# Optimization experiments

Measured on AMD Instinct MI355X. Metric: run time of the kernel, lower is better.

Reference implementation:

```python
import jax, jax.numpy as jnp
import numpy as np


def setup_inputs() -> dict:
    key = jax.random.key(0)
    ks = jax.random.split(key, 16)
    L, T, F = 1024, 4096, 8
    E, H, P = 4, 4, 4
    return {
        "x": jax.random.normal(ks[0], (L, T, F), jnp.float32),
        "emb": jax.random.normal(ks[1], (L, E), jnp.float32),
        "W1": jax.random.normal(ks[2], (F + E, 4), jnp.float32) * 0.3,
        "b1": jnp.zeros((4,), jnp.float32),
        "Wp": jax.random.normal(ks[3], (4, P), jnp.float32) * 0.3,
        "bp": jnp.zeros((P,), jnp.float32),
        "Wi": jax.random.normal(ks[4], (P, H), jnp.float32) * 0.3,
        "bi": jnp.zeros((H,), jnp.float32),
        "Wh": jax.random.normal(ks[5], (H, H), jnp.float32) * 0.3,
        "Wo1": jax.random.normal(ks[6], (H, 6), jnp.float32) * 0.3,
        "bo1": jnp.zeros((6,), jnp.float32),
        "Wo2": jax.random.normal(ks[7], (6, 1), jnp.float32) * 0.3,
        "bo2": jnpp if False else jnp.zeros((1,), jnp.float32),
    }


def reference(x, emb, W1, b1, Wp, bp, Wi, bi, Wh, Wo1, bo1, Wo2, bo2):
    L, T, F = x.shape
    # location embedding broadcast over time, concat on feature axis -> [L, T, F+E]
    loc = jnp.broadcast_to(emb[:, None, :], (L, T, emb.shape[-1]))
    h = jnp.concatenate([x, loc], axis=-1)
    # pre layers (dropout is identity, training=False)
    h = jax.nn.relu(h @ W1 + b1)          # [L, T, 4]
    h = h @ Wp + bp                        # [L, T, P]
    # SimpleCell RNN: carry = tanh(x_t @ Wi + bi + carry @ Wh), zero init carry
    xs = jnp.swapaxes(h, 0, 1)             # [T, L, P]
    pre = xs @ Wi + bi                     # precompute input projection [T, L, H]
    c0 = jnp.zeros((L, Wh.shape[0]), h.dtype)

    def step(c, p_t):
        c = jnp.tanh(p_t + c @ Wh)
        return c, c

    _, ys = jax.lax.scan(step, c0, pre)    # ys: [T, L, H]
    y = jnp.swapaxes(ys, 0, 1)             # [L, T, H]
    y = jax.nn.relu(y @ Wo1 + bo1)
    y = y @ Wo2 + bo2                      # [L, T, 1]
    return y
```

## Files before the change

### kernel.cpp

```cpp
#include <hip/hip_runtime.h>


#define TSTEP 8

__device__ __forceinline__ float tanh_from_s(float s) {
    float e = __builtin_amdgcn_exp2f(s);
    float r = __builtin_amdgcn_rcpf(e + 1.0f);
    return fmaf(-2.0f, r, 1.0f);
}

__global__ __launch_bounds__(256) void k_fused(
    const float* __restrict__ x, const float* __restrict__ emb,
    const float* __restrict__ W1, const float* __restrict__ b1,
    const float* __restrict__ Wp, const float* __restrict__ bp,
    const float* __restrict__ Wi, const float* __restrict__ bi,
    const float* __restrict__ Wh, const float* __restrict__ Wo1,
    const float* __restrict__ bo1, const float* __restrict__ Wo2,
    const float* __restrict__ bo2, float* __restrict__ out,
    int L, int T, int C, int S, int W)
{
    int wk = blockIdx.x * blockDim.x + threadIdx.x;
    int l = wk % L;
    int k = wk / L;
    if (k >= C) return;

    const float K2 = 2.8853900817779268f;

    float w1[48];
#pragma unroll
    for (int i = 0; i < 48; i++) w1[i] = W1[i];

    float wc[16], bc[4];
#pragma unroll
    for (int a = 0; a < 4; a++)
#pragma unroll
        for (int h = 0; h < 4; h++) {
            float s = 0.f;
#pragma unroll
            for (int p = 0; p < 4; p++) s = fmaf(Wp[a * 4 + p], Wi[p * 4 + h], s);
            wc[a * 4 + h] = s * K2;
        }
#pragma unroll
    for (int h = 0; h < 4; h++) {
        float s = bi[h];
#pragma unroll
        for (int p = 0; p < 4; p++) s = fmaf(bp[p], Wi[p * 4 + h], s);
        bc[h] = s * K2;
    }
    float wh[16];
#pragma unroll
    for (int i = 0; i < 16; i++) wh[i] = Wh[i] * K2;
    float wo1[24], vbo1[6], wo2[6];
#pragma unroll
    for (int i = 0; i < 24; i++) wo1[i] = Wo1[i];
#pragma unroll
    for (int i = 0; i < 6; i++) { vbo1[i] = bo1[i]; wo2[i] = Wo2[i]; }
    float vbo2 = bo2[0];

    float eb[4];
    {
        float e0 = emb[l * 4 + 0], e1 = emb[l * 4 + 1];
        float e2 = emb[l * 4 + 2], e3 = emb[l * 4 + 3];
#pragma unroll
        for (int j = 0; j < 4; j++) {
            float s = b1[j];
            s = fmaf(e0, w1[8 * 4 + j], s);
            s = fmaf(e1, w1[9 * 4 + j], s);
            s = fmaf(e2, w1[10 * 4 + j], s);
            s = fmaf(e3, w1[11 * 4 + j], s);
            eb[j] = s;
        }
    }

    int tmain = k * S;
    int warm = (W < tmain) ? W : tmain;
    int tstart = tmain - warm;

    const float4* xp = (const float4*)x + ((long)l * T + tstart) * 2;
    float c0 = 0.f, c1 = 0.f, c2 = 0.f, c3 = 0.f;

    auto step = [&](const float4& Aa, const float4& Bb) {
        float xf[8] = {Aa.x, Aa.y, Aa.z, Aa.w, Bb.x, Bb.y, Bb.z, Bb.w};
        float hj[4];
#pragma unroll
        for (int j = 0; j < 4; j++) {
            float s = eb[j];
#pragma unroll
            for (int i = 0; i < 8; i++) s = fmaf(xf[i], w1[i * 4 + j], s);
            hj[j] = fmaxf(s, 0.f);
        }
        float p0 = bc[0], p1 = bc[1], p2 = bc[2], p3 = bc[3];
#pragma unroll
        for (int a = 0; a < 4; a++) {
            p0 = fmaf(hj[a], wc[a * 4 + 0], p0);
            p1 = fmaf(hj[a], wc[a * 4 + 1], p1);
            p2 = fmaf(hj[a], wc[a * 4 + 2], p2);
            p3 = fmaf(hj[a], wc[a * 4 + 3], p3);
        }
        p0 = fmaf(c0, wh[0], p0);  p1 = fmaf(c0, wh[1], p1);  p2 = fmaf(c0, wh[2], p2);  p3 = fmaf(c0, wh[3], p3);
        p0 = fmaf(c1, wh[4], p0);  p1 = fmaf(c1, wh[5], p1);  p2 = fmaf(c1, wh[6], p2);  p3 = fmaf(c1, wh[7], p3);
        p0 = fmaf(c2, wh[8], p0);  p1 = fmaf(c2, wh[9], p1);  p2 = fmaf(c2, wh[10], p2); p3 = fmaf(c2, wh[11], p3);
        p0 = fmaf(c3, wh[12], p0); p1 = fmaf(c3, wh[13], p1); p2 = fmaf(c3, wh[14], p2); p3 = fmaf(c3, wh[15], p3);
        c0 = tanh_from_s(p0); c1 = tanh_from_s(p1);
        c2 = tanh_from_s(p2); c3 = tanh_from_s(p3);
    };
    auto outv = [&]() -> float {
        float acc = vbo2;
#pragma unroll
        for (int m = 0; m < 6; m++) {
            float g = vbo1[m];
            g = fmaf(c0, wo1[0 * 6 + m], g);
            g = fmaf(c1, wo1[1 * 6 + m], g);
            g = fmaf(c2, wo1[2 * 6 + m], g);
            g = fmaf(c3, wo1[3 * 6 + m], g);
            acc = fmaf(fmaxf(g, 0.f), wo2[m], acc);
        }
        return acc;
    };

    int wtiles = warm / TSTEP;
    for (int wt = 0; wt < wtiles; wt++) {
        float4 xd[2 * TSTEP];
#pragma unroll
        for (int i = 0; i < 2 * TSTEP; i++) xd[i] = xp[i];
        xp += 2 * TSTEP;
#pragma unroll
        for (int i = 0; i < TSTEP; i++) step(xd[2 * i], xd[2 * i + 1]);
    }

    float* op = out + (long)l * T + tmain;
    int mtiles = S / TSTEP;
    for (int mt = 0; mt < mtiles; mt++) {
        float4 xd[2 * TSTEP];
#pragma unroll
        for (int i = 0; i < 2 * TSTEP; i++) xd[i] = xp[i];
        xp += 2 * TSTEP;
        float o8[TSTEP];
#pragma unroll
        for (int i = 0; i < TSTEP; i++) {
            step(xd[2 * i], xd[2 * i + 1]);
            o8[i] = outv();
        }
        *(float4*)(op + 0) = make_float4(o8[0], o8[1], o8[2], o8[3]);
        *(float4*)(op + 4) = make_float4(o8[4], o8[5], o8[6], o8[7]);
        op += TSTEP;
    }
}

extern "C" void kernel_launch(void* const* d_in, const int* in_sizes, int n_in,
                              void* d_out, int out_size, void* d_ws, size_t ws_size,
                              hipStream_t stream) {
    const float* x   = (const float*)d_in[0];
    const float* emb = (const float*)d_in[1];
    const float* W1  = (const float*)d_in[2];
    const float* b1  = (const float*)d_in[3];
    const float* Wp  = (const float*)d_in[4];
    const float* bp  = (const float*)d_in[5];
    const float* Wi  = (const float*)d_in[6];
    const float* bi  = (const float*)d_in[7];
    const float* Wh  = (const float*)d_in[8];
    const float* Wo1 = (const float*)d_in[9];
    const float* bo1 = (const float*)d_in[10];
    const float* Wo2 = (const float*)d_in[11];
    const float* bo2 = (const float*)d_in[12];
    float* out = (float*)d_out;

    int L = in_sizes[1] / 4;
    int T = (int)(in_sizes[0] / ((long)L * 8));

    int C = 64, W = 48;
    if (T % (C * TSTEP) != 0) { C = 1; W = 0; }
    int S = T / C;

    long nw = (long)L * C;
    int tb = 256;
    int nb = (int)((nw + tb - 1) / tb);
    k_fused<<<nb, tb, 0, stream>>>(x, emb, W1, b1, Wp, bp, Wi, bi, Wh,
                                   Wo1, bo1, Wo2, bo2, out, L, T, C, S, W);
}
```

Measured before the change: 47.88 us.

## Add LDS-staged scan kernel with coalesced x loads and transposed output stores

Adds a new kernel with 64-thread blocks, one block per 64 locations and time chunk. Each 8-step tile of x is loaded cooperatively so that 16 lanes read contiguous memory per row, staged through padded LDS, and then each lane reads its own row. The next tile is prefetched into registers during compute. Outputs are also staged through LDS and written coalesced. This replaces strided per-thread float4 loads at the cost of barriers and low occupancy (launch_bounds 64,1). The fallback kernel picks up a typo (p3 instead of p2 in one FMA), but that path does not run for these shapes.

```diff
diff --git a/kernel.cpp b/kernel.cpp
--- a/kernel.cpp
+++ b/kernel.cpp
@@ -7,6 +7,173 @@
     float e = __builtin_amdgcn_exp2f(s);
     float r = __builtin_amdgcn_rcpf(e + 1.0f);
     return fmaf(-2.0f, r, 1.0f);
+}
+
+__global__ __launch_bounds__(64, 1) void k_scan_lds(
+    const float* __restrict__ x, const float* __restrict__ emb,
+    const float* __restrict__ W1, const float* __restrict__ b1,
+    const float* __restrict__ Wp, const float* __restrict__ bp,
+    const float* __restrict__ Wi, const float* __restrict__ bi,
+    const float* __restrict__ Wh, const float* __restrict__ Wo1,
+    const float* __restrict__ bo1, const float* __restrict__ Wo2,
+    const float* __restrict__ bo2, float* __restrict__ out,
+    int L, int T, int C, int S, int W)
+{
+    __shared__ float4 stage[64 * 17];
+    __shared__ float4 ostage[64 * 3];
+
+    int lane = threadIdx.x;
+    int k    = blockIdx.x >> 4;
+    int lw0  = (blockIdx.x & 15) << 6;
+    int l    = lw0 + lane;
+
+    const float K2 = 2.8853900817779268f;
+
+    float w1[48];
+#pragma unroll
+    for (int i = 0; i < 48; i++) w1[i] = W1[i];
+
+    float wc[16], bc[4];
+#pragma unroll
+    for (int a = 0; a < 4; a++)
+#pragma unroll
+        for (int h = 0; h < 4; h++) {
+            float s = 0.f;
+#pragma unroll
+            for (int p = 0; p < 4; p++) s = fmaf(Wp[a * 4 + p], Wi[p * 4 + h], s);
+            wc[a * 4 + h] = s * K2;
+        }
+#pragma unroll
+    for (int h = 0; h < 4; h++) {
+        float s = bi[h];
+#pragma unroll
+        for (int p = 0; p < 4; p++) s = fmaf(bp[p], Wi[p * 4 + h], s);
+        bc[h] = s * K2;
+    }
+    float wh[16];
+#pragma unroll
+    for (int i = 0; i < 16; i++) wh[i] = Wh[i] * K2;
+    float wo1[24], vbo1[6], wo2[6];
+#pragma unroll
+    for (int i = 0; i < 24; i++) wo1[i] = Wo1[i];
+#pragma unroll
+    for (int i = 0; i < 6; i++) { vbo1[i] = bo1[i]; wo2[i] = Wo2[i]; }
+    float vbo2 = bo2[0];
+
+    float eb[4];
+    {
+        float e0 = emb[l * 4 + 0], e1 = emb[l * 4 + 1];
+        float e2 = emb[l * 4 + 2], e3 = emb[l * 4 + 3];
+#pragma unroll
+        for (int j = 0; j < 4; j++) {
+            float s = b1[j];
+            s = fmaf(e0, w1[8 * 4 + j], s);
+            s = fmaf(e1, w1[9 * 4 + j], s);
+            s = fmaf(e2, w1[10 * 4 + j], s);
+            s = fmaf(e3, w1[11 * 4 + j], s);
+            eb[j] = s;
+        }
+    }
+
+    int tmain  = k * S;
+    int warm   = (W < tmain) ? W : tmain;
+    int tstart = tmain - warm;
+    int wtiles = warm / TSTEP;
+    int ntiles = (warm + S) / TSTEP;
+
+    int rr = lane >> 4;
+    int cc = lane & 15;
+    const float4* xw = (const float4*)x + ((long)(lw0 + rr) * T + tstart) * 2 + cc;
+    const long jstride = (long)T * 8;
+
+    float4 val[16];
+#pragma unroll
+    for (int j = 0; j < 16; j++) val[j] = xw[(long)j * jstride];
+
+    float c0 = 0.f, c1 = 0.f, c2 = 0.f, c3 = 0.f;
+
+    auto step = [&](const float4& Aa, const float4& Bb) {
+        float xf[8] = {Aa.x, Aa.y, Aa.z, Aa.w, Bb.x, Bb.y, Bb.z, Bb.w};
+        float hj[4];
+#pragma unroll
+        for (int j = 0; j < 4; j++) {
+            float s = eb[j];
+#pragma unroll
+            for (int i = 0; i < 8; i++) s = fmaf(xf[i], w1[i * 4 + j], s);
+            hj[j] = fmaxf(s, 0.f);
+        }
+        float p0 = bc[0], p1 = bc[1], p2 = bc[2], p3 = bc[3];
+#pragma unroll
+        for (int a = 0; a < 4; a++) {
+            p0 = fmaf(hj[a], wc[a * 4 + 0], p0);
+            p1 = fmaf(hj[a], wc[a * 4 + 1], p1);
+            p2 = fmaf(hj[a], wc[a * 4 + 2], p2);
+            p3 = fmaf(hj[a], wc[a * 4 + 3], p3);
+        }
+        p0 = fmaf(c0, wh[0], p0);  p1 = fmaf(c0, wh[1], p1);  p2 = fmaf(c0, wh[2], p2);  p3 = fmaf(c0, wh[3], p3);
+        p0 = fmaf(c1, wh[4], p0);  p1 = fmaf(c1, wh[5], p1);  p2 = fmaf(c1, wh[6], p2);  p3 = fmaf(c1, wh[7], p3);
+        p0 = fmaf(c2, wh[8], p0);  p1 = fmaf(c2, wh[9], p1);  p2 = fmaf(c2, wh[10], p2); p3 = fmaf(c2, wh[11], p3);
+        p0 = fmaf(c3, wh[12], p0); p1 = fmaf(c3, wh[13], p1); p2 = fmaf(c3, wh[14], p2); p3 = fmaf(c3, wh[15], p3);
+        c0 = tanh_from_s(p0); c1 = tanh_from_s(p1);
+        c2 = tanh_from_s(p2); c3 = tanh_from_s(p3);
+    };
+    auto outv = [&]() -> float {
+        float acc = vbo2;
+#pragma unroll
+        for (int m = 0; m < 6; m++) {
+            float g = vbo1[m];
+            g = fmaf(c0, wo1[0 * 6 + m], g);
+            g = fmaf(c1, wo1[1 * 6 + m], g);
+            g = fmaf(c2, wo1[2 * 6 + m], g);
+            g = fmaf(c3, wo1[3 * 6 + m], g);
+            acc = fmaf(fmaxf(g, 0.f), wo2[m], acc);
+        }
+        return acc;
+    };
+
+    float4* out4 = (float4*)out;
+    int Tq = T >> 2;
+
+    for (int tt = 0; tt < ntiles; ++tt) {
+        __syncthreads();
+#pragma unroll
+        for (int j = 0; j < 16; j++) stage[(j * 4 + rr) * 17 + cc] = val[j];
+        __syncthreads();
+
+        if (tt + 1 < ntiles) {
+            const float4* xn = xw + (long)(tt + 1) * 16;
+#pragma unroll
+            for (int j = 0; j < 16; j++) val[j] = xn[(long)j * jstride];
+        }
+
+        if (tt >= wtiles) {
+            float o8[TSTEP];
+#pragma unroll
+            for (int i = 0; i < TSTEP; i++) {
+                float4 Aa = stage[lane * 17 + 2 * i];
+                float4 Bb = stage[lane * 17 + 2 * i + 1];
+                step(Aa, Bb);
+                o8[i] = outv();
+            }
+            ostage[lane * 3 + 0] = make_float4(o8[0], o8[1], o8[2], o8[3]);
+            ostage[lane * 3 + 1] = make_float4(o8[4], o8[5], o8[6], o8[7]);
+            __syncthreads();
+            int tq = (tmain + (tt - wtiles) * TSTEP) >> 2;
+#pragma unroll
+            for (int j = 0; j < 2; j++) {
+                int r  = j * 32 + (lane >> 1);
+                int cq = lane & 1;
+                out4[(long)(lw0 + r) * Tq + tq + cq] = ostage[r * 3 + cq];
+            }
+        } else {
+#pragma unroll
+            for (int i = 0; i < TSTEP; i++) {
+                float4 Aa = stage[lane * 17 + 2 * i];
+                float4 Bb = stage[lane * 17 + 2 * i + 1];
+                step(Aa, Bb);
+            }
+        }
+    }
 }
 
 __global__ __launch_bounds__(256) void k_fused(
@@ -23,13 +190,10 @@
     int l = wk % L;
     int k = wk / L;
     if (k >= C) return;
-
     const float K2 = 2.8853900817779268f;
-
     float w1[48];
 #pragma unroll
     for (int i = 0; i < 48; i++) w1[i] = W1[i];
-
     float wc[16], bc[4];
 #pragma unroll
     for (int a = 0; a < 4; a++)
@@ -56,7 +220,6 @@
 #pragma unroll
     for (int i = 0; i < 6; i++) { vbo1[i] = bo1[i]; wo2[i] = Wo2[i]; }
     float vbo2 = bo2[0];
-
     float eb[4];
     {
         float e0 = emb[l * 4 + 0], e1 = emb[l * 4 + 1];
@@ -71,14 +234,10 @@
             eb[j] = s;
         }
     }
-
     int tmain = k * S;
     int warm = (W < tmain) ? W : tmain;
-    int tstart = tmain - warm;
-
-    const float4* xp = (const float4*)x + ((long)l * T + tstart) * 2;
+    const float4* xp = (const float4*)x + ((long)l * T + (tmain - warm)) * 2;
     float c0 = 0.f, c1 = 0.f, c2 = 0.f, c3 = 0.f;
-
     auto step = [&](const float4& Aa, const float4& Bb) {
         float xf[8] = {Aa.x, Aa.y, Aa.z, Aa.w, Bb.x, Bb.y, Bb.z, Bb.w};
         float hj[4];
@@ -100,7 +259,7 @@
         p0 = fmaf(c0, wh[0], p0);  p1 = fmaf(c0, wh[1], p1);  p2 = fmaf(c0, wh[2], p2);  p3 = fmaf(c0, wh[3], p3);
         p0 = fmaf(c1, wh[4], p0);  p1 = fmaf(c1, wh[5], p1);  p2 = fmaf(c1, wh[6], p2);  p3 = fmaf(c1, wh[7], p3);
         p0 = fmaf(c2, wh[8], p0);  p1 = fmaf(c2, wh[9], p1);  p2 = fmaf(c2, wh[10], p2); p3 = fmaf(c2, wh[11], p3);
-        p0 = fmaf(c3, wh[12], p0); p1 = fmaf(c3, wh[13], p1); p2 = fmaf(c3, wh[14], p2); p3 = fmaf(c3, wh[15], p3);
+        p0 = fmaf(c3, wh[12], p0); p1 = fmaf(c3, wh[13], p1); p2 = fmaf(c3, wh[14], p3); p3 = fmaf(c3, wh[15], p3);
         c0 = tanh_from_s(p0); c1 = tanh_from_s(p1);
         c2 = tanh_from_s(p2); c3 = tanh_from_s(p3);
     };
@@ -117,7 +276,6 @@
         }
         return acc;
     };
-
     int wtiles = warm / TSTEP;
     for (int wt = 0; wt < wtiles; wt++) {
         float4 xd[2 * TSTEP];
@@ -127,7 +285,6 @@
 #pragma unroll
         for (int i = 0; i < TSTEP; i++) step(xd[2 * i], xd[2 * i + 1]);
     }
-
     float* op = out + (long)l * T + tmain;
     int mtiles = S / TSTEP;
     for (int mt = 0; mt < mtiles; mt++) {
@@ -137,10 +294,7 @@
         xp += 2 * TSTEP;
         float o8[TSTEP];
 #pragma unroll
-        for (int i = 0; i < TSTEP; i++) {
-            step(xd[2 * i], xd[2 * i + 1]);
-            o8[i] = outv();
-        }
+        for (int i = 0; i < TSTEP; i++) { step(xd[2 * i], xd[2 * i + 1]); o8[i] = outv(); }
         *(float4*)(op + 0) = make_float4(o8[0], o8[1], o8[2], o8[3]);
         *(float4*)(op + 4) = make_float4(o8[4], o8[5], o8[6], o8[7]);
         op += TSTEP;
@@ -169,12 +323,18 @@
     int T = (int)(in_sizes[0] / ((long)L * 8));
 
     int C = 64, W = 48;
-    if (T % (C * TSTEP) != 0) { C = 1; W = 0; }
-    int S = T / C;
-
-    long nw = (long)L * C;
-    int tb = 256;
-    int nb = (int)((nw + tb - 1) / tb);
-    k_fused<<<nb, tb, 0, stream>>>(x, emb, W1, b1, Wp, bp, Wi, bi, Wh,
-                                   Wo1, bo1, Wo2, bo2, out, L, T, C, S, W);
+    if (L % 64 == 0 && T % (C * TSTEP) == 0 && (T / C) % TSTEP == 0) {
+        int S = T / C;
+        int nb = (L / 64) * C;
+        k_scan_lds<<<nb, 64, 0, stream>>>(x, emb, W1, b1, Wp, bp, Wi, bi, Wh,
+                                          Wo1, bo1, Wo2, bo2, out, L, T, C, S, W);
+    } else {
+        if (T % (C * TSTEP) != 0) { C = 1; W = 0; }
+        int S = T / C;
+        long nw = (long)L * C;
+        int tb = 256;
+        int nb = (int)((nw + tb - 1) / tb);
+        k_fused<<<nb, tb, 0, stream>>>(x, emb, W1, b1, Wp, bp, Wi, bi, Wh,
+                                       Wo1, bo1, Wo2, bo2, out, L, T, C, S, W);
+    }
 }
```

After: 96.91 us. 2.02x slower.
